# Kernel tuning notes

Hardware: AMD Instinct MI355X
Metric: run time of the kernel (lower is better)

The kernel has to match this reference:

```python
import jax, jax.numpy as jnp
import numpy as np

N = 20000   # nodes
E = 320000  # edges
F = 64      # input node features
H = 256     # hidden_layer_size
C = 10      # nbr_classes
G = 64      # graphs in the batch


def _lin(key, fan_in, fan_out):
    k1, k2 = jax.random.split(key)
    bound = 1.0 / np.sqrt(fan_in)
    W = jax.random.uniform(k1, (fan_in, fan_out), jnp.float32, -bound, bound)
    b = jax.random.uniform(k2, (fan_out,), jnp.float32, -bound, bound)
    return W, b


def setup_inputs() -> dict:
    key = jax.random.key(0)
    ks = jax.random.split(key, 10)
    x = jax.random.normal(ks[0], (N, F), jnp.float32)
    edge_index = jax.random.randint(ks[1], (2, E), 0, N)
    batch = jnp.sort(jax.random.randint(ks[2], (N,), 0, G))
    W1, b1 = _lin(ks[3], F, H)
    W2, b2 = _lin(ks[4], H, H)
    W3, b3 = _lin(ks[5], H, H)
    W4, b4 = _lin(ks[6], H, H)
    W5, b5 = _lin(ks[7], H, H)
    Wout, bout = _lin(ks[8], H, C)
    return {"x": x, "edge_index": edge_index, "batch": batch,
            "W1": W1, "b1": b1, "W2": W2, "b2": b2, "W3": W3, "b3": b3,
            "W4": W4, "b4": b4, "W5": W5, "b5": b5, "Wout": Wout, "bout": bout}


def reference(x, edge_index, batch, W1, b1, W2, b2, W3, b3, W4, b4, W5, b5, Wout, bout):
    # GCNConv (Kipf & Welling): add self-loops, D^{-1/2}(A+I)D^{-1/2} (X W) + b.
    # Dropout(p=0.5) is identity in eval mode (reference is deterministic).
    loop = jnp.arange(N)
    row = jnp.concatenate([edge_index[0], loop])  # source nodes, [E+N]
    col = jnp.concatenate([edge_index[1], loop])  # target nodes, [E+N]
    deg = jax.ops.segment_sum(jnp.ones(E + N, x.dtype), col, num_segments=N)
    dinv = jax.lax.rsqrt(deg)  # deg >= 1 thanks to self-loops
    norm = (dinv[row] * dinv[col])[:, None]  # [E+N, 1]

    def gcn_conv(h, W, b):
        m = (h @ W)[row] * norm                      # gather + normalize, [E+N, H]
        return jax.ops.segment_sum(m, col, num_segments=N) + b

    h = x
    for W, b in ((W1, b1), (W2, b2), (W3, b3), (W4, b4), (W5, b5)):
        h = jax.nn.relu(gcn_conv(h, W, b))

    # global_mean_pool over graph ids
    counts = jax.ops.segment_sum(jnp.ones(N, h.dtype), batch, num_segments=G)
    pooled = jax.ops.segment_sum(h, batch, num_segments=G) / jnp.maximum(counts, 1.0)[:, None]
    return pooled @ Wout + bout  # [G, C]
```

## Files before the change

kernel.cpp:

```cpp
#include <hip/hip_runtime.h>

#define NN 20000
#define NE 320000
#define FIN 64
#define HD 256
#define NC 10
#define NG 64
#define NB ((NN + 255) / 256)
#define EBMAX (NE + 15 * NN + 16)

typedef unsigned short u16;
typedef unsigned int u32;
typedef __attribute__((ext_vector_type(8))) short short8;
typedef __attribute__((ext_vector_type(4))) float f32x4;

__device__ __forceinline__ float bf2f(u16 u) {
    union { u32 i; float f; } v; v.i = ((u32)u) << 16; return v.f;
}
__device__ __forceinline__ u16 f2bf(float f) {
    union { float f; u32 i; } v; v.f = f;
    u32 r = v.i + 0x7fffu + ((v.i >> 16) & 1u);
    return (u16)(r >> 16);
}

__global__ void k_deg(const int* __restrict__ col, int* __restrict__ degi,
                      const int* __restrict__ batch, int* __restrict__ gstart) {
    int i = blockIdx.x * 256 + threadIdx.x;
    if (i < NE) atomicAdd(&degi[col[i]], 1);
    if (i < NN) {
        int b = batch[i];
        int prev = (i == 0) ? -1 : batch[i - 1];
        if (b != prev) gstart[b] = i;
    }
}

__global__ void k_pad(u32* __restrict__ ebuf32) {
    int i = blockIdx.x * 256 + threadIdx.x;
    if (i < EBMAX / 2) ebuf32[i] = 0x4E204E20u;
}

__global__ __launch_bounds__(256) void k_scan1(const int* __restrict__ degi,
                                               int* __restrict__ rowptr,
                                               int* __restrict__ bsum) {
    int t = threadIdx.x;
    int i = blockIdx.x * 256 + t;
    int v = (i < NN) ? ((degi[i] + 15) & ~15) : 0;
    int lane = t & 63, wid = t >> 6;
    int x = v;
#pragma unroll
    for (int off = 1; off < 64; off <<= 1) {
        int y = __shfl_up(x, off);
        if (lane >= off) x += y;
    }
    __shared__ int ws[4];
    if (lane == 63) ws[wid] = x;
    __syncthreads();
    int woff = 0;
    for (int w = 0; w < wid; ++w) woff += ws[w];
    if (i < NN) rowptr[i] = woff + x - v;
    if (t == 255) bsum[blockIdx.x] = woff + x;
}

__global__ void k_scan3(const int* __restrict__ degi, const int* __restrict__ bsum,
                        int* __restrict__ rowptr, int* __restrict__ cursor,
                        float* __restrict__ dinv,
                        const float* __restrict__ x, u16* __restrict__ u0) {
    __shared__ int pref[NB];
    if (threadIdx.x < NB) pref[threadIdx.x] = bsum[threadIdx.x];
    __syncthreads();
    if (threadIdx.x == 0) {
        int run = 0;
        for (int k = 0; k < NB; ++k) { int t = pref[k]; pref[k] = run; run += t; }
    }
    __syncthreads();
    int i = blockIdx.x * 256 + threadIdx.x;
    if (i < NN) {
        int dg = degi[i];
        int rp = rowptr[i] + pref[i >> 8];
        rowptr[i] = rp;
        cursor[i] = rp;
        dinv[i] = rsqrtf((float)(1 + dg));
        if (i == NN - 1) rowptr[NN] = rp + ((dg + 15) & ~15);
    }
    if (i < NN * FIN / 4) {
        int node = i >> 4;
        float d = rsqrtf((float)(1 + degi[node]));
        float4 v = *(const float4*)&x[(size_t)i * 4];
        u32 lo = (u32)f2bf(v.x * d) | ((u32)f2bf(v.y * d) << 16);
        u32 hi = (u32)f2bf(v.z * d) | ((u32)f2bf(v.w * d) << 16);
        *(uint2*)&u0[(size_t)i * 4] = make_uint2(lo, hi);
    }
    if (blockIdx.x == 0 && threadIdx.x < FIN) u0[(size_t)NN * FIN + threadIdx.x] = 0;
}

__global__ void k_fill(const int* __restrict__ row, const int* __restrict__ col,
                       int* __restrict__ cursor, u16* __restrict__ ebuf) {
    int e = blockIdx.x * 256 + threadIdx.x;
    if (e < NE) {
        int c = col[e];
        int pos = atomicAdd(&cursor[c], 1);
        ebuf[pos] = (u16)row[e];
    }
}

__global__ __launch_bounds__(256) void k_trans(const float* __restrict__ W0, const float* __restrict__ W1,
                                               const float* __restrict__ W2, const float* __restrict__ W3,
                                               const float* __restrict__ W4,
                                               u16* __restrict__ T0, u16* __restrict__ T1,
                                               u16* __restrict__ T2, u16* __restrict__ T3,
                                               u16* __restrict__ T4) {
    int l = blockIdx.z;
    const float* W = (l == 0) ? W0 : (l == 1) ? W1 : (l == 2) ? W2 : (l == 3) ? W3 : W4;
    u16* T = (l == 0) ? T0 : (l == 1) ? T1 : (l == 2) ? T2 : (l == 3) ? T3 : T4;
    int K = (l == 0) ? FIN : HD;
    int k0 = blockIdx.x * 32;
    if (k0 >= K) return;
    int n0 = blockIdx.y * 32;
    __shared__ float tile[32][33];
    int tx = threadIdx.x & 31, ty = threadIdx.x >> 5;
#pragma unroll
    for (int r = 0; r < 32; r += 8)
        tile[ty + r][tx] = W[(size_t)(k0 + ty + r) * HD + n0 + tx];
    __syncthreads();
#pragma unroll
    for (int r = 0; r < 32; r += 8)
        T[(size_t)(n0 + ty + r) * K + k0 + tx] = f2bf(tile[tx][ty + r]);
}

__global__ __launch_bounds__(512, 8) void k_fused(const u16* __restrict__ U,
                                                  const int* __restrict__ rowptr,
                                                  const u16* __restrict__ ebuf,
                                                  const float* __restrict__ dinv,
                                                  const u16* __restrict__ Wt,
                                                  const float* __restrict__ bias,
                                                  u16* __restrict__ O,
                                                  int K, int scaleOut) {
    __shared__ u16 Asm[16][264];
    __shared__ u16 Bsm[256][40];
    __shared__ float bs[HD];
    const int m0 = blockIdx.x * 16;
    const int t = threadIdx.x;
    const int wave = t >> 6;
    const int lane = t & 63;
    if (t < HD) bs[t] = bias[t];
    if (blockIdx.x == 0 && t < HD) O[(size_t)NN * HD + t] = 0;

    if (K == HD) {
        const int grp = lane >> 4;
        const int seg = lane & 15;
        for (int task = wave; task < 32; task += 8) {
            const int row = task >> 1;
            const int n = m0 + row;
            const int fbase = (task & 1) * 128 + seg * 8;
            const int s = rowptr[n], e = rowptr[n + 1];
            float acc[8];
            if (grp == 0) {
                uint4 v = *(const uint4*)&U[(size_t)n * HD + fbase];
                acc[0] = bf2f((u16)(v.x & 0xffff)); acc[1] = bf2f((u16)(v.x >> 16));
                acc[2] = bf2f((u16)(v.y & 0xffff)); acc[3] = bf2f((u16)(v.y >> 16));
                acc[4] = bf2f((u16)(v.z & 0xffff)); acc[5] = bf2f((u16)(v.z >> 16));
                acc[6] = bf2f((u16)(v.w & 0xffff)); acc[7] = bf2f((u16)(v.w >> 16));
            } else {
#pragma unroll
                for (int k = 0; k < 8; ++k) acc[k] = 0.f;
            }
            for (int j = s; j < e; j += 16) {
                int myid = (lane < 16) ? (int)ebuf[j + lane] : 0;
                uint4 v[4];
#pragma unroll
                for (int k = 0; k < 4; ++k) {
                    int r = __shfl(myid, grp * 4 + k);
                    v[k] = *(const uint4*)&U[(size_t)r * HD + fbase];
                }
#pragma unroll
                for (int k = 0; k < 4; ++k) {
                    acc[0] += bf2f((u16)(v[k].x & 0xffff)); acc[1] += bf2f((u16)(v[k].x >> 16));
                    acc[2] += bf2f((u16)(v[k].y & 0xffff)); acc[3] += bf2f((u16)(v[k].y >> 16));
                    acc[4] += bf2f((u16)(v[k].z & 0xffff)); acc[5] += bf2f((u16)(v[k].z >> 16));
                    acc[6] += bf2f((u16)(v[k].w & 0xffff)); acc[7] += bf2f((u16)(v[k].w >> 16));
                }
            }
#pragma unroll
            for (int k = 0; k < 8; ++k) {
                acc[k] += __shfl_xor(acc[k], 16);
                acc[k] += __shfl_xor(acc[k], 32);
            }
            if (grp == 0) {
                float d = dinv[n];
                uint4 o;
                o.x = (u32)f2bf(acc[0] * d) | ((u32)f2bf(acc[1] * d) << 16);
                o.y = (u32)f2bf(acc[2] * d) | ((u32)f2bf(acc[3] * d) << 16);
                o.z = (u32)f2bf(acc[4] * d) | ((u32)f2bf(acc[5] * d) << 16);
                o.w = (u32)f2bf(acc[6] * d) | ((u32)f2bf(acc[7] * d) << 16);
                *(uint4*)&Asm[row][fbase] = o;
            }
        }
    } else {
        const int grp = lane >> 3;
        const int seg = lane & 7;
        for (int task = wave; task < 16; task += 8) {
            const int n = m0 + task;
            const int s = rowptr[n], e = rowptr[n + 1];
            float acc[8];
            if (grp == 0) {
                uint4 v = *(const uint4*)&U[(size_t)n * FIN + seg * 8];
                acc[0] = bf2f((u16)(v.x & 0xffff)); acc[1] = bf2f((u16)(v.x >> 16));
                acc[2] = bf2f((u16)(v.y & 0xffff)); acc[3] = bf2f((u16)(v.y >> 16));
                acc[4] = bf2f((u16)(v.z & 0xffff)); acc[5] = bf2f((u16)(v.z >> 16));
                acc[6] = bf2f((u16)(v.w & 0xffff)); acc[7] = bf2f((u16)(v.w >> 16));
            } else {
#pragma unroll
                for (int k = 0; k < 8; ++k) acc[k] = 0.f;
            }
            for (int j = s; j < e; j += 16) {
                int r0 = (int)ebuf[j + grp];
                int r1 = (int)ebuf[j + 8 + grp];
                uint4 v0 = *(const uint4*)&U[(size_t)r0 * FIN + seg * 8];
                uint4 v1 = *(const uint4*)&U[(size_t)r1 * FIN + seg * 8];
                acc[0] += bf2f((u16)(v0.x & 0xffff)); acc[1] += bf2f((u16)(v0.x >> 16));
                acc[2] += bf2f((u16)(v0.y & 0xffff)); acc[3] += bf2f((u16)(v0.y >> 16));
                acc[4] += bf2f((u16)(v0.z & 0xffff)); acc[5] += bf2f((u16)(v0.z >> 16));
                acc[6] += bf2f((u16)(v0.w & 0xffff)); acc[7] += bf2f((u16)(v0.w >> 16));
                acc[0] += bf2f((u16)(v1.x & 0xffff)); acc[1] += bf2f((u16)(v1.x >> 16));
                acc[2] += bf2f((u16)(v1.y & 0xffff)); acc[3] += bf2f((u16)(v1.y >> 16));
                acc[4] += bf2f((u16)(v1.z & 0xffff)); acc[5] += bf2f((u16)(v1.z >> 16));
                acc[6] += bf2f((u16)(v1.w & 0xffff)); acc[7] += bf2f((u16)(v1.w >> 16));
            }
#pragma unroll
            for (int off = 8; off < 64; off <<= 1)
#pragma unroll
                for (int k = 0; k < 8; ++k) acc[k] += __shfl_xor(acc[k], off);
            if (grp == 0) {
                float d = dinv[n];
                uint4 o;
                o.x = (u32)f2bf(acc[0] * d) | ((u32)f2bf(acc[1] * d) << 16);
                o.y = (u32)f2bf(acc[2] * d) | ((u32)f2bf(acc[3] * d) << 16);
                o.z = (u32)f2bf(acc[4] * d) | ((u32)f2bf(acc[5] * d) << 16);
                o.w = (u32)f2bf(acc[6] * d) | ((u32)f2bf(acc[7] * d) << 16);
                *(uint4*)&Asm[task][seg * 8] = o;
            }
        }
    }
    __syncthreads();

    const int quad = lane >> 4;
    const int l16 = lane & 15;
    const int n0 = wave * 32;
    f32x4 acc[2];
#pragma unroll
    for (int j = 0; j < 2; ++j) acc[j] = (f32x4){0.f, 0.f, 0.f, 0.f};

    for (int k0 = 0; k0 < K; k0 += 32) {
        {
            int r = t >> 1, h16 = (t & 1) * 16;
#pragma unroll
            for (int j = 0; j < 2; ++j) {
                float4 v = *(const float4*)&Wt[(size_t)r * K + k0 + h16 + j * 8];
                *(float4*)&Bsm[r][h16 + j * 8] = v;
            }
        }
        __syncthreads();
        short8 a = *(const short8*)&Asm[l16][k0 + quad * 8];
        short8 b[2];
#pragma unroll
        for (int j = 0; j < 2; ++j) b[j] = *(const short8*)&Bsm[n0 + j * 16 + l16][quad * 8];
#pragma unroll
        for (int j = 0; j < 2; ++j)
            acc[j] = __builtin_amdgcn_mfma_f32_16x16x32_bf16(a, b[j], acc[j], 0, 0, 0);
        __syncthreads();
    }
#pragma unroll
    for (int r = 0; r < 4; ++r) {
        int m = m0 + quad * 4 + r;
        float d = scaleOut ? dinv[m] : 1.0f;
#pragma unroll
        for (int j = 0; j < 2; ++j) {
            int n = n0 + j * 16 + l16;
            float val = fmaxf(acc[j][r] + bs[n], 0.f) * d;
            O[(size_t)m * HD + n] = f2bf(val);
        }
    }
}

__global__ __launch_bounds__(256) void k_poolout(const u16* __restrict__ h,
                                                 const int* __restrict__ gstart,
                                                 const float* __restrict__ Wout,
                                                 const float* __restrict__ bout,
                                                 float* __restrict__ out) {
    int g = blockIdx.x;
    int t = threadIdx.x;
    __shared__ float pooled[HD];
    __shared__ float part[NC][16];
    __shared__ int s_se[2];
    if (t == 0) {
        int st = gstart[g];
        int en = NN;
        for (int gg = g + 1; gg < NG; ++gg) en = min(en, gstart[gg]);
        s_se[0] = st; s_se[1] = en;
    }
    __syncthreads();
    int st = s_se[0], en = s_se[1];
    float a0 = 0.f, a1 = 0.f, a2 = 0.f, a3 = 0.f;
    int n = st;
    for (; n + 4 <= en; n += 4) {
        a0 += bf2f(h[(size_t)n * HD + t]);
        a1 += bf2f(h[(size_t)(n + 1) * HD + t]);
        a2 += bf2f(h[(size_t)(n + 2) * HD + t]);
        a3 += bf2f(h[(size_t)(n + 3) * HD + t]);
    }
    for (; n < en; ++n) a0 += bf2f(h[(size_t)n * HD + t]);
    float inv = 1.0f / (float)max(en - st, 1);
    pooled[t] = (a0 + a1 + a2 + a3) * inv;
    __syncthreads();
    if (t < NC * 16) {
        int c = t >> 4, l16 = t & 15;
        float s = 0.f;
        for (int f = l16; f < HD; f += 16)
            s = fmaf(pooled[f], Wout[(size_t)f * NC + c], s);
        part[c][l16] = s;
    }
    __syncthreads();
    if (t < NC) {
        float s = 0.f;
#pragma unroll
        for (int k = 0; k < 16; ++k) s += part[t][k];
        out[(size_t)g * NC + t] = s + bout[t];
    }
}

extern "C" void kernel_launch(void* const* d_in, const int* in_sizes, int n_in,
                              void* d_out, int out_size, void* d_ws, size_t ws_size,
                              hipStream_t stream) {
    const float* x     = (const float*)d_in[0];
    const int*   ei    = (const int*)d_in[1];
    const int*   batch = (const int*)d_in[2];
    const float* Wl[5] = {(const float*)d_in[3], (const float*)d_in[5], (const float*)d_in[7],
                          (const float*)d_in[9], (const float*)d_in[11]};
    const float* bl[5] = {(const float*)d_in[4], (const float*)d_in[6], (const float*)d_in[8],
                          (const float*)d_in[10], (const float*)d_in[12]};
    const float* Wout = (const float*)d_in[13];
    const float* bout = (const float*)d_in[14];
    float* out = (float*)d_out;

    const int* row = ei;
    const int* col = ei + NE;

    char* p = (char*)d_ws;
    auto take = [&](size_t bytes) { char* q = p; p += (bytes + 255) & ~(size_t)255; return q; };
    float* dinv   = (float*)take(NN * 4);
    int*   degi   = (int*)take(NN * 4);
    int*   rowptr = (int*)take((NN + 1) * 4);
    int*   cursor = (int*)take(NN * 4);
    int*   bsum   = (int*)take(NB * 4);
    u16*   ebuf   = (u16*)take(EBMAX * 2);
    int*   gstart = (int*)take(NG * 4);
    u16*   Wt[5];
    for (int l = 0; l < 5; ++l) Wt[l] = (u16*)take((size_t)HD * HD * 2);
    u16*   B1     = (u16*)take((size_t)(NN + 1) * HD * 2);
    u16*   B2     = (u16*)take((size_t)(NN + 1) * HD * 2);

    hipMemsetAsync(degi, 0, NN * 4, stream);
    hipMemsetAsync(gstart, 0x7F, NG * 4, stream);
    k_deg<<<(NE + 255) / 256, 256, 0, stream>>>(col, degi, batch, gstart);
    k_pad<<<(EBMAX / 2 + 255) / 256, 256, 0, stream>>>((u32*)ebuf);
    k_scan1<<<NB, 256, 0, stream>>>(degi, rowptr, bsum);
    k_scan3<<<(NN * FIN / 4 + 255) / 256, 256, 0, stream>>>(degi, bsum, rowptr, cursor, dinv, x, B1);
    k_fill<<<(NE + 255) / 256, 256, 0, stream>>>(row, col, cursor, ebuf);
    dim3 tGrid(8, 8, 5);
    k_trans<<<tGrid, 256, 0, stream>>>(Wl[0], Wl[1], Wl[2], Wl[3], Wl[4],
                                       Wt[0], Wt[1], Wt[2], Wt[3], Wt[4]);

    const int fGrid = NN / 16;
    k_fused<<<fGrid, 512, 0, stream>>>(B1, rowptr, ebuf, dinv, Wt[0], bl[0], B2, FIN, 1);
    k_fused<<<fGrid, 512, 0, stream>>>(B2, rowptr, ebuf, dinv, Wt[1], bl[1], B1, HD, 1);
    k_fused<<<fGrid, 512, 0, stream>>>(B1, rowptr, ebuf, dinv, Wt[2], bl[2], B2, HD, 1);
    k_fused<<<fGrid, 512, 0, stream>>>(B2, rowptr, ebuf, dinv, Wt[3], bl[3], B1, HD, 1);
    k_fused<<<fGrid, 512, 0, stream>>>(B1, rowptr, ebuf, dinv, Wt[4], bl[4], B2, HD, 0);

    k_poolout<<<NG, 256, 0, stream>>>(B2, gstart, Wout, bout, out);
}
```

Before: 333.5 us.

## Read weights directly from global in MFMA loop, merge pad kernel, widen pooling

The GEMM stage of the fused GCN kernel drops its shared-memory B tile and the two barriers per k-step, loading transposed bf16 weights straight from global (L2-resident) into MFMA operands. The gather loop now reads four edge indices per lane-group with one vector load instead of a lane load followed by shuffles, and the task-to-row mapping is reordered. The degree and pad kernels are merged into one launch, and pooling uses 512 threads split across alternating nodes. The trade is more global/L2 traffic for the weight operand in exchange for less LDS use and no block syncs, which could raise occupancy.

```diff
diff --git a/kernel.cpp b/kernel.cpp
--- a/kernel.cpp
+++ b/kernel.cpp
@@ -23,8 +23,9 @@
     return (u16)(r >> 16);
 }
 
-__global__ void k_deg(const int* __restrict__ col, int* __restrict__ degi,
-                      const int* __restrict__ batch, int* __restrict__ gstart) {
+__global__ void k_degpad(const int* __restrict__ col, int* __restrict__ degi,
+                         const int* __restrict__ batch, int* __restrict__ gstart,
+                         u32* __restrict__ ebuf32) {
     int i = blockIdx.x * 256 + threadIdx.x;
     if (i < NE) atomicAdd(&degi[col[i]], 1);
     if (i < NN) {
@@ -32,10 +33,6 @@
         int prev = (i == 0) ? -1 : batch[i - 1];
         if (b != prev) gstart[b] = i;
     }
-}
-
-__global__ void k_pad(u32* __restrict__ ebuf32) {
-    int i = blockIdx.x * 256 + threadIdx.x;
     if (i < EBMAX / 2) ebuf32[i] = 0x4E204E20u;
 }
 
@@ -136,7 +133,6 @@
                                                   u16* __restrict__ O,
                                                   int K, int scaleOut) {
     __shared__ u16 Asm[16][264];
-    __shared__ u16 Bsm[256][40];
     __shared__ float bs[HD];
     const int m0 = blockIdx.x * 16;
     const int t = threadIdx.x;
@@ -148,10 +144,11 @@
     if (K == HD) {
         const int grp = lane >> 4;
         const int seg = lane & 15;
-        for (int task = wave; task < 32; task += 8) {
-            const int row = task >> 1;
+        for (int tk = 0; tk < 4; ++tk) {
+            const int task = wave + tk * 8;
+            const int row = task & 15;
             const int n = m0 + row;
-            const int fbase = (task & 1) * 128 + seg * 8;
+            const int fbase = (task >> 4) * 128 + seg * 8;
             const int s = rowptr[n], e = rowptr[n + 1];
             float acc[8];
             if (grp == 0) {
@@ -165,13 +162,14 @@
                 for (int k = 0; k < 8; ++k) acc[k] = 0.f;
             }
             for (int j = s; j < e; j += 16) {
-                int myid = (lane < 16) ? (int)ebuf[j + lane] : 0;
+                uint2 idv = *(const uint2*)&ebuf[j + grp * 4];
+                int r0 = (int)(idv.x & 0xffff), r1 = (int)(idv.x >> 16);
+                int r2 = (int)(idv.y & 0xffff), r3 = (int)(idv.y >> 16);
                 uint4 v[4];
-#pragma unroll
-                for (int k = 0; k < 4; ++k) {
-                    int r = __shfl(myid, grp * 4 + k);
-                    v[k] = *(const uint4*)&U[(size_t)r * HD + fbase];
-                }
+                v[0] = *(const uint4*)&U[(size_t)r0 * HD + fbase];
+                v[1] = *(const uint4*)&U[(size_t)r1 * HD + fbase];
+                v[2] = *(const uint4*)&U[(size_t)r2 * HD + fbase];
+                v[3] = *(const uint4*)&U[(size_t)r3 * HD + fbase];
 #pragma unroll
                 for (int k = 0; k < 4; ++k) {
                     acc[0] += bf2f((u16)(v[k].x & 0xffff)); acc[1] += bf2f((u16)(v[k].x >> 16));
@@ -250,24 +248,13 @@
 #pragma unroll
     for (int j = 0; j < 2; ++j) acc[j] = (f32x4){0.f, 0.f, 0.f, 0.f};
 
+#pragma unroll 2
     for (int k0 = 0; k0 < K; k0 += 32) {
-        {
-            int r = t >> 1, h16 = (t & 1) * 16;
-#pragma unroll
-            for (int j = 0; j < 2; ++j) {
-                float4 v = *(const float4*)&Wt[(size_t)r * K + k0 + h16 + j * 8];
-                *(float4*)&Bsm[r][h16 + j * 8] = v;
-            }
-        }
-        __syncthreads();
         short8 a = *(const short8*)&Asm[l16][k0 + quad * 8];
-        short8 b[2];
-#pragma unroll
-        for (int j = 0; j < 2; ++j) b[j] = *(const short8*)&Bsm[n0 + j * 16 + l16][quad * 8];
-#pragma unroll
-        for (int j = 0; j < 2; ++j)
-            acc[j] = __builtin_amdgcn_mfma_f32_16x16x32_bf16(a, b[j], acc[j], 0, 0, 0);
-        __syncthreads();
+        short8 b0 = *(const short8*)&Wt[(size_t)(n0 + l16) * K + k0 + quad * 8];
+        short8 b1 = *(const short8*)&Wt[(size_t)(n0 + 16 + l16) * K + k0 + quad * 8];
+        acc[0] = __builtin_amdgcn_mfma_f32_16x16x32_bf16(a, b0, acc[0], 0, 0, 0);
+        acc[1] = __builtin_amdgcn_mfma_f32_16x16x32_bf16(a, b1, acc[1], 0, 0, 0);
     }
 #pragma unroll
     for (int r = 0; r < 4; ++r) {
@@ -282,13 +269,16 @@
     }
 }
 
-__global__ __launch_bounds__(256) void k_poolout(const u16* __restrict__ h,
+__global__ __launch_bounds__(512) void k_poolout(const u16* __restrict__ h,
                                                  const int* __restrict__ gstart,
                                                  const float* __restrict__ Wout,
                                                  const float* __restrict__ bout,
                                                  float* __restrict__ out) {
     int g = blockIdx.x;
     int t = threadIdx.x;
+    int f = t & (HD - 1);
+    int half = t >> 8;
+    __shared__ float pp[2][HD];
     __shared__ float pooled[HD];
     __shared__ float part[NC][16];
     __shared__ int s_se[2];
@@ -301,22 +291,26 @@
     __syncthreads();
     int st = s_se[0], en = s_se[1];
     float a0 = 0.f, a1 = 0.f, a2 = 0.f, a3 = 0.f;
-    int n = st;
-    for (; n + 4 <= en; n += 4) {
-        a0 += bf2f(h[(size_t)n * HD + t]);
-        a1 += bf2f(h[(size_t)(n + 1) * HD + t]);
-        a2 += bf2f(h[(size_t)(n + 2) * HD + t]);
-        a3 += bf2f(h[(size_t)(n + 3) * HD + t]);
-    }
-    for (; n < en; ++n) a0 += bf2f(h[(size_t)n * HD + t]);
-    float inv = 1.0f / (float)max(en - st, 1);
-    pooled[t] = (a0 + a1 + a2 + a3) * inv;
+    int n = st + half;
+    for (; n + 6 < en; n += 8) {
+        a0 += bf2f(h[(size_t)n * HD + f]);
+        a1 += bf2f(h[(size_t)(n + 2) * HD + f]);
+        a2 += bf2f(h[(size_t)(n + 4) * HD + f]);
+        a3 += bf2f(h[(size_t)(n + 6) * HD + f]);
+    }
+    for (; n < en; n += 2) a0 += bf2f(h[(size_t)n * HD + f]);
+    pp[half][f] = a0 + a1 + a2 + a3;
+    __syncthreads();
+    if (t < HD) {
+        float inv = 1.0f / (float)max(en - st, 1);
+        pooled[t] = (pp[0][t] + pp[1][t]) * inv;
+    }
     __syncthreads();
     if (t < NC * 16) {
         int c = t >> 4, l16 = t & 15;
         float s = 0.f;
-        for (int f = l16; f < HD; f += 16)
-            s = fmaf(pooled[f], Wout[(size_t)f * NC + c], s);
+        for (int ff = l16; ff < HD; ff += 16)
+            s = fmaf(pooled[ff], Wout[(size_t)ff * NC + c], s);
         part[c][l16] = s;
     }
     __syncthreads();
@@ -361,8 +355,7 @@
 
     hipMemsetAsync(degi, 0, NN * 4, stream);
     hipMemsetAsync(gstart, 0x7F, NG * 4, stream);
-    k_deg<<<(NE + 255) / 256, 256, 0, stream>>>(col, degi, batch, gstart);
-    k_pad<<<(EBMAX / 2 + 255) / 256, 256, 0, stream>>>((u32*)ebuf);
+    k_degpad<<<(NE + 255) / 256, 256, 0, stream>>>(col, degi, batch, gstart, (u32*)ebuf);
     k_scan1<<<NB, 256, 0, stream>>>(degi, rowptr, bsum);
     k_scan3<<<(NN * FIN / 4 + 255) / 256, 256, 0, stream>>>(degi, bsum, rowptr, cursor, dinv, x, B1);
     k_fill<<<(NE + 255) / 256, 256, 0, stream>>>(row, col, cursor, ebuf);
@@ -377,5 +370,5 @@
     k_fused<<<fGrid, 512, 0, stream>>>(B2, rowptr, ebuf, dinv, Wt[3], bl[3], B1, HD, 1);
     k_fused<<<fGrid, 512, 0, stream>>>(B1, rowptr, ebuf, dinv, Wt[4], bl[4], B2, HD, 0);
 
-    k_poolout<<<NG, 256, 0, stream>>>(B2, gstart, Wout, bout, out);
-}
+    k_poolout<<<NG, 512, 0, stream>>>(B2, gstart, Wout, bout, out);
+}
```

New measurement: 367.6 us. +10.2%, slower.
